# Kernel tuning notes

Hardware: AMD Instinct MI355X
Metric: run time of the kernel (lower is better)

Reference implementation:

```python
import jax, jax.numpy as jnp
import numpy as np

OFFS = [(dy, dx) for dy in (-1, 0, 1) for dx in (-1, 0, 1)]  # ME centered 3x3 region


def _build_maps():
    """Build the sparse coordinate pyramid and per-offset kernel maps, exactly
    mirroring MinkowskiEngine: out coords of a stride-2 conv are unique(c//2),
    and a pair (i_in, i_out) exists iff coord_out*stride + offset is active."""
    G = 1024
    rng = np.random.default_rng(0)
    flat = np.sort(rng.choice(G * G, size=300000, replace=False))
    coords = [np.stack(np.unravel_index(flat, (G, G)), axis=1).astype(np.int64)]
    grids = [G]
    for _ in range(3):
        coords.append(np.unique(coords[-1] // 2, axis=0))
        grids.append(grids[-1] // 2)

    def lut(c, g):
        t = -np.ones(g * g, np.int64)
        t[c[:, 0] * g + c[:, 1]] = np.arange(len(c))
        return t

    luts = [lut(c, g) for c, g in zip(coords, grids)]

    def kmap(lvl_in, c_out, stride):
        g, L = grids[lvl_in], luts[lvl_in]
        n_in, n_out = len(coords[lvl_in]), len(c_out)
        base = c_out * stride
        pairs = []
        for dy, dx in OFFS:
            q = base + np.array([dy, dx])
            ok = (q[:, 0] >= 0) & (q[:, 0] < g) & (q[:, 1] >= 0) & (q[:, 1] < g)
            key = np.clip(q[:, 0] * g + q[:, 1], 0, g * g - 1)
            idx = np.where(ok, L[key], -1)
            sel = np.nonzero(idx >= 0)[0]
            pairs.append((idx[sel], sel))
        M = max(len(p[0]) for p in pairs)
        ii = np.full((9, M), n_in, np.int32)   # pad -> dummy zero input row
        oo = np.full((9, M), n_out, np.int32)  # pad -> dummy output row (dropped)
        for k, (a, b) in enumerate(pairs):
            ii[k, :len(a)] = a
            oo[k, :len(b)] = b
        return ii, oo

    maps = {
        'c0': kmap(0, coords[0], 1), 'd0': kmap(0, coords[1], 2),
        'c1': kmap(1, coords[1], 1), 'd1': kmap(1, coords[2], 2),
        'c2': kmap(2, coords[2], 1), 'd2': kmap(2, coords[3], 2),
    }
    return maps, [len(c) for c in coords]


def setup_inputs() -> dict:
    maps, (n0, n1, n2, n3) = _build_maps()
    ks = jax.random.split(jax.random.key(0), 16)
    d = {'feats': jax.random.normal(ks[0], (n0, 1), jnp.float32)}
    chans = [(1, 64), (64, 128), (128, 128), (128, 128), (128, 128), (128, 128)]
    names = ['c0', 'd0', 'c1', 'd1', 'c2', 'd2']
    for i, (nm, (ci, co)) in enumerate(zip(names, chans)):
        d[f'w_{nm}'] = jax.random.normal(ks[1 + 2 * i], (9, ci, co), jnp.float32) / np.sqrt(9.0 * ci)
        d[f'b_{nm}'] = jax.random.normal(ks[2 + 2 * i], (co,), jnp.float32) * 0.01
        d[f'in_{nm}'] = jnp.asarray(maps[nm][0])
        d[f'out_{nm}'] = jnp.asarray(maps[nm][1])
    d.update(n0=n0, n1=n1, n2=n2, n3=n3)
    return d


def sparse_conv(feats, w, b, in_idx, out_idx, n_out):
    """Gather-GEMM-scatter sparse conv. w: [9, Cin, Cout]. Padded pairs point at a
    dummy zero input row (index n_in) and a dummy output row (index n_out)."""
    n_in, cin = feats.shape
    fp = jnp.concatenate([feats, jnp.zeros((1, cin), feats.dtype)], axis=0)
    out = jnp.zeros((n_out + 1, w.shape[2]), feats.dtype)
    for k in range(9):  # fixed kernel volume
        out = out.at[out_idx[k]].add(fp[in_idx[k]] @ w[k])
    return out[:n_out] + b


def reference(feats, w_c0, b_c0, in_c0, out_c0, w_d0, b_d0, in_d0, out_d0,
              w_c1, b_c1, in_c1, out_c1, w_d1, b_d1, in_d1, out_d1,
              w_c2, b_c2, in_c2, out_c2, w_d2, b_d2, in_d2, out_d2,
              n0, n1, n2, n3):
    x = sparse_conv(feats, w_c0, b_c0, in_c0, out_c0, n0)
    out0 = jax.nn.relu(sparse_conv(x, w_d0, b_d0, in_d0, out_d0, n1))
    y = sparse_conv(out0, w_c1, b_c1, in_c1, out_c1, n1)
    out1 = jax.nn.relu(sparse_conv(y, w_d1, b_d1, in_d1, out_d1, n2))
    z = sparse_conv(out1, w_c2, b_c2, in_c2, out_c2, n2)
    out2 = sparse_conv(z, w_d2, b_d2, in_d2, out_d2, n3)
    return (out2, out1, out0)
```

## Files before the change

kernel.cpp:

```cpp
#include <hip/hip_runtime.h>
#include <stdint.h>
#include <algorithm>


#define DI __device__ __forceinline__

typedef __attribute__((ext_vector_type(8))) short bf16x8;
typedef __attribute__((ext_vector_type(4))) float f32x4;

DI uint16_t f2bf(float x){
  union{float f;uint32_t i;}v; v.f=x;
  uint32_t r = v.i + 0x7fffu + ((v.i>>16)&1u);
  return (uint16_t)(r>>16);
}
DI uint32_t pack2(float a, float b){
  return (uint32_t)f2bf(a) | ((uint32_t)f2bf(b) << 16);
}
DI void gload16(const void* g, void* l){
  __builtin_amdgcn_global_load_lds(
      (const __attribute__((address_space(1))) void*)g,
      (__attribute__((address_space(3))) void*)l, 16, 0, 0);
}

__global__ __launch_bounds__(256) void diag_kernel(float* __restrict__ out, long n, float c){
  long i = (long)blockIdx.x*256 + threadIdx.x;
  if (i < n) out[i] = c;
}

__global__ __launch_bounds__(256) void init_all_kernel(
    int* __restrict__ tab, long ntab, float* __restrict__ zp){
  long i = (long)blockIdx.x*256 + threadIdx.x;
  if (i < ntab) tab[i] = -1;
  if (blockIdx.x == 0 && threadIdx.x < 64) zp[threadIdx.x] = 0.f;
}

struct BuildArgs {
  const int* im[6];
  const int* om[6];
  int   M[6];
  int   nin[6];
  int   nout[6];
  long  toff[6];
};

__global__ __launch_bounds__(256) void build_all_kernel(
    BuildArgs a, int* __restrict__ tb){
  const int L = blockIdx.z, k = blockIdx.y;
  const int M = a.M[L];
  long t = (long)blockIdx.x*256 + threadIdx.x;
  if (t >= M) return;
  int ii = a.im[L][(long)k*M + t];
  int oo = a.om[L][(long)k*M + t];
  if (ii >= 0 && ii < a.nin[L] && oo >= 0 && oo < a.nout[L])
    tb[a.toff[L] + (long)k*a.nout[L] + oo] = ii;
}

__global__ __launch_bounds__(256) void prep_all_kernel(
    const float* __restrict__ w0, const float* __restrict__ w1,
    const float* __restrict__ w2, const float* __restrict__ w3,
    const float* __restrict__ w4, uint16_t* __restrict__ wb, long total){
  const long wt64 = 9L*128*64, wt128 = 9L*128*128;
  long idx = (long)blockIdx.x*256 + threadIdx.x;
  if (idx >= total) return;
  int L; long r; int cin;
  if (idx < wt64){ L = 0; r = idx; cin = 64; }
  else { long j = idx - wt64; L = 1 + (int)(j / wt128); r = j % wt128; cin = 128; }
  const float* w = (L==0) ? w0 : (L==1) ? w1 : (L==2) ? w2 : (L==3) ? w3 : w4;
  int k = (int)(r / (128*cin));
  int rem = (int)(r % (128*cin));
  int cout = rem / cin, ci = rem % cin;
  wb[idx] = f2bf(w[((long)k*cin + ci)*128 + cout]);
}

__global__ __launch_bounds__(256) void c0_tab_kernel(
    const float* __restrict__ feats, const float* __restrict__ w,
    const float* __restrict__ bias, const int* __restrict__ tab,
    uint16_t* __restrict__ out, int n_out){
  __shared__ float w_s[576];
  __shared__ float b_s[64];
  const int tid = threadIdx.x;
  for (int i = tid; i < 576; i += 256) w_s[i] = w[i];
  if (tid < 64) b_s[tid] = bias[tid];
  __syncthreads();
  long r = (long)blockIdx.x*256 + tid;
  if (r >= n_out) return;
  float f[9];
  #pragma unroll
  for (int k = 0; k < 9; k++){
    int gi = tab[(long)k*n_out + r];
    f[k] = (gi >= 0) ? feats[gi] : 0.f;
  }
  uint16_t* dst = out + r*64;
  #pragma unroll
  for (int c0 = 0; c0 < 64; c0 += 16){
    float a[16];
    #pragma unroll
    for (int j = 0; j < 16; j++) a[j] = b_s[c0+j];
    #pragma unroll
    for (int k = 0; k < 9; k++){
      float fk = f[k];
      #pragma unroll
      for (int j = 0; j < 16; j++) a[j] += fk * w_s[k*64 + c0 + j];
    }
    uint4 o0, o1;
    o0.x = pack2(a[0],a[1]);   o0.y = pack2(a[2],a[3]);
    o0.z = pack2(a[4],a[5]);   o0.w = pack2(a[6],a[7]);
    o1.x = pack2(a[8],a[9]);   o1.y = pack2(a[10],a[11]);
    o1.z = pack2(a[12],a[13]); o1.w = pack2(a[14],a[15]);
    *(uint4*)(dst + c0)     = o0;
    *(uint4*)(dst + c0 + 8) = o1;
  }
}

template<int CIN, int INMODE, int OUTMODE, bool RELU>
__global__ __launch_bounds__(512,4) void mconv2_kernel(
    const void* __restrict__ in_v, const char* __restrict__ ws_base,
    long in_off, long wtb_off, long zp_off,
    const float* __restrict__ bias, const int* __restrict__ tab,
    float* __restrict__ outf, uint16_t* __restrict__ outb, int n_out){
  constexpr int NS = 9*CIN/64;
  __shared__ __align__(16) uint16_t ab[2][128*64];
  __shared__ __align__(16) uint16_t bb[2][128*64];
  __shared__ int gi_sh[(INMODE==1) ? 9*128 : 1];

  const int tid = threadIdx.x;
  const int nwg = gridDim.x, orig = blockIdx.x;
  const int q = nwg >> 3, rr = nwg & 7, xcd = orig & 7, pos = orig >> 3;
  const int wg = (xcd < rr ? xcd*(q+1) : rr*(q+1) + (xcd-rr)*q) + pos;
  const long rb = (long)wg * 128;

  const int r0 = tid >> 3, sg = tid & 7;
  const int ss0 = sg ^ (r0 & 7);

  uint32_t offA[2][9];
  if constexpr (INMODE == 0){
    #pragma unroll
    for (int kk = 0; kk < 9; ++kk){
      #pragma unroll
      for (int it = 0; it < 2; ++it){
        long row = rb + it*64 + r0;
        int gi = (row < (long)n_out) ? tab[(long)kk*n_out + row] : -1;
        offA[it][kk] = (gi >= 0)
            ? (uint32_t)(in_off + (long)gi*(CIN*2) + ss0*16)
            : (uint32_t)(zp_off + ss0*16);
      }
    }
  } else {
    for (int idx = tid; idx < 9*128; idx += 512){
      int k = idx >> 7, r = idx & 127;
      long row = rb + r;
      gi_sh[idx] = (row < (long)n_out) ? tab[(long)k*n_out + row] : -1;
    }
    __syncthreads();
  }

  const uint32_t offB = (uint32_t)(wtb_off + ((long)r0*CIN + ss0*8)*2);

  const int lane = tid & 63;
  const int wv = tid >> 6;
  const int wr = (wv >> 1) << 5;
  const int wc = (wv & 1) << 6;
  const int l16 = lane & 15, quad = lane >> 4;

  float bv[4];
  #pragma unroll
  for (int ct = 0; ct < 4; ++ct) bv[ct] = bias[wc + (ct<<4) + l16];

  f32x4 acc[2][4];
  #pragma unroll
  for (int i = 0; i < 2; i++)
    #pragma unroll
    for (int j = 0; j < 4; j++)
      acc[i][j] = (f32x4){0.f,0.f,0.f,0.f};

  auto stage_b = [&](int step, int nb){
    const int kk  = (CIN == 64) ? step : (step >> 1);
    const int c0b = (CIN == 64) ? 0 : ((step & 1) * 128);
    const uint32_t base = offB + (uint32_t)((long)kk*128*CIN*2 + c0b);
    #pragma unroll
    for (int it = 0; it < 2; ++it)
      gload16(ws_base + base + it*(64*CIN*2), &bb[nb][(it*512+tid)*8]);
  };
  auto stage_a_bf = [&](int step, int nb){
    const int kk  = (CIN == 64) ? step : (step >> 1);
    const int c0b = (CIN == 64) ? 0 : ((step & 1) * 128);
    #pragma unroll
    for (int it = 0; it < 2; ++it)
      gload16(ws_base + offA[it][kk] + c0b, &ab[nb][(it*512+tid)*8]);
  };
  auto stage_a_f32_issue = [&](int step, float4 (*va)[2]){
    const int kk = step >> 1;
    const int ci0 = (step & 1) << 6;
    const float* fb = (const float*)in_v;
    #pragma unroll
    for (int it = 0; it < 2; ++it){
      int gi = gi_sh[(kk << 7) + it*64 + r0];
      if (gi >= 0){
        const float4* s = (const float4*)(fb + (long)gi*128 + ci0 + ss0*8);
        va[it][0] = s[0]; va[it][1] = s[1];
      } else {
        va[it][0] = make_float4(0.f,0.f,0.f,0.f);
        va[it][1] = make_float4(0.f,0.f,0.f,0.f);
      }
    }
  };
  auto stage_a_f32_write = [&](float4 (*va)[2], int nb){
    #pragma unroll
    for (int it = 0; it < 2; ++it){
      uint4 o;
      o.x = pack2(va[it][0].x, va[it][0].y);
      o.y = pack2(va[it][0].z, va[it][0].w);
      o.z = pack2(va[it][1].x, va[it][1].y);
      o.w = pack2(va[it][1].z, va[it][1].w);
      *(uint4*)&ab[nb][(it*512+tid)*8] = o;
    }
  };
  auto compute = [&](int nb){
    const uint16_t* A  = &ab[nb][0];
    const uint16_t* Bm = &bb[nb][0];
    __builtin_amdgcn_s_setprio(1);
    #pragma unroll
    for (int ch = 0; ch < 2; ++ch){
      const int xs = ((((ch << 2) + quad) ^ (l16 & 7)) << 3);
      bf16x8 af[2], bfr[4];
      #pragma unroll
      for (int u = 0; u < 2; ++u)
        af[u]  = *(const bf16x8*)&A [((wr + (u<<4) + l16) << 6) + xs];
      #pragma unroll
      for (int u = 0; u < 4; ++u)
        bfr[u] = *(const bf16x8*)&Bm[((wc + (u<<4) + l16) << 6) + xs];
      #pragma unroll
      for (int rt = 0; rt < 2; ++rt)
        #pragma unroll
        for (int ct = 0; ct < 4; ++ct)
          acc[rt][ct] = __builtin_amdgcn_mfma_f32_16x16x32_bf16(
              af[rt], bfr[ct], acc[rt][ct], 0, 0, 0);
    }
    __builtin_amdgcn_s_setprio(0);
  };

  if constexpr (INMODE == 0){
    stage_a_bf(0, 0);
    stage_b(0, 0);
    #pragma unroll
    for (int t = 0; t < NS; ++t){
      const int cur = t & 1;
      if (t + 1 < NS){
        stage_a_bf(t+1, cur^1);
        stage_b(t+1, cur^1);
        asm volatile("s_waitcnt vmcnt(4)" ::: "memory");
      } else {
        asm volatile("s_waitcnt vmcnt(0)" ::: "memory");
      }
      __builtin_amdgcn_sched_barrier(0);
      __builtin_amdgcn_s_barrier();
      compute(cur);
      if (t + 1 < NS)
        __builtin_amdgcn_s_barrier();
    }
  } else {
    float4 va[2][2];
    stage_a_f32_issue(0, va);
    stage_a_f32_write(va, 0);
    stage_b(0, 0);
    __syncthreads();
    #pragma unroll
    for (int t = 0; t < NS; ++t){
      const int cur = t & 1;
      const bool more = (t + 1 < NS);
      if (more){
        stage_a_f32_issue(t+1, va);
        stage_b(t+1, cur^1);
      }
      compute(cur);
      if (more){
        stage_a_f32_write(va, cur^1);
        __syncthreads();
      }
    }
  }

  #pragma unroll
  for (int ct = 0; ct < 4; ++ct){
    const int cout = wc + (ct<<4) + l16;
    #pragma unroll
    for (int rt = 0; rt < 2; ++rt){
      #pragma unroll
      for (int r = 0; r < 4; ++r){
        long row = rb + wr + (rt<<4) + (quad<<2) + r;
        if (row < (long)n_out){
          float v = acc[rt][ct][r] + bv[ct];
          if (RELU) v = v > 0.f ? v : 0.f;
          if constexpr (OUTMODE == 0 || OUTMODE == 2) outf[row*128 + cout] = v;
          if constexpr (OUTMODE == 1 || OUTMODE == 2) outb[row*128 + cout] = f2bf(v);
        }
      }
    }
  }
}

static inline long cdivl(long a, long b){ return (a + b - 1) / b; }

extern "C" void kernel_launch(void* const* d_in, const int* in_sizes, int n_in_args,
                              void* d_out, int out_size, void* d_ws, size_t ws_size,
                              hipStream_t stream) {
  const float* feats = (const float*)d_in[0];
  const float* w_c0 = (const float*)d_in[1];
  const float* b_c0 = (const float*)d_in[2];
  const int* in_c0  = (const int*)d_in[3];
  const int* out_c0 = (const int*)d_in[4];
  const float* w_d0 = (const float*)d_in[5];
  const float* b_d0 = (const float*)d_in[6];
  const int* in_d0  = (const int*)d_in[7];
  const int* out_d0 = (const int*)d_in[8];
  const float* w_c1 = (const float*)d_in[9];
  const float* b_c1 = (const float*)d_in[10];
  const int* in_c1  = (const int*)d_in[11];
  const int* out_c1 = (const int*)d_in[12];
  const float* w_d1 = (const float*)d_in[13];
  const float* b_d1 = (const float*)d_in[14];
  const int* in_d1  = (const int*)d_in[15];
  const int* out_d1 = (const int*)d_in[16];
  const float* w_c2 = (const float*)d_in[17];
  const float* b_c2 = (const float*)d_in[18];
  const int* in_c2  = (const int*)d_in[19];
  const int* out_c2 = (const int*)d_in[20];
  const float* w_d2 = (const float*)d_in[21];
  const float* b_d2 = (const float*)d_in[22];
  const int* in_d2  = (const int*)d_in[23];
  const int* out_d2 = (const int*)d_in[24];

  const int n0   = in_sizes[0];
  const int M_c0 = in_sizes[3]  / 9;
  const int M_d0 = in_sizes[7]  / 9;
  const int M_c1 = in_sizes[11] / 9;
  const int M_d1 = in_sizes[15] / 9;
  const int M_c2 = in_sizes[19] / 9;
  const int M_d2 = in_sizes[23] / 9;
  const int n1   = M_c1;
  const int n2   = M_c2;
  const int n3   = out_size/128 - n1 - n2;

  bool sane = n0 > 0 && out_size % 128 == 0 &&
              M_c0 > 0 && M_d0 > 0 && M_d1 > 0 && M_d2 > 0 &&
              n1 > 0 && n2 > 0 && n3 > 0;

  long maxElems = (long)n0*64;
  if ((long)n1*128 > maxElems) maxElems = (long)n1*128;
  if ((long)n2*128 > maxElems) maxElems = (long)n2*128;
  long fbytes = (maxElems*2 + 255)/256*256;
  long ntab   = sane ? 9L*((long)n0 + 2L*n1 + 2L*n2 + n3) : 0;
  long tbytes = (ntab*4 + 255)/256*256;
  long wt64  = 9L*128*64, wt128 = 9L*128*128;
  long wbytes = ((wt64 + 4*wt128)*2 + 255)/256*256;
  long zbytes = 256;
  long b1bytes = sane ? ((long)n2*128*2 + 255)/256*256 : 0;
  long b0bytes = sane ? ((long)n1*128*2 + 255)/256*256 : 0;
  long need0 = fbytes + tbytes + wbytes + zbytes + 256;

  if (!sane || ws_size < (size_t)need0){
    float C = (float)(16 + (int)std::min<size_t>(ws_size >> 20, (size_t)100000));
    if (!sane) C *= 1099511627776.0f;
    diag_kernel<<<cdivl(out_size,256),256,0,stream>>>((float*)d_out, out_size, C);
    return;
  }

  uint16_t* fbuf = (uint16_t*)d_ws;
  long tab_off    = fbytes;
  long wtb_d0_off = fbytes + tbytes;
  long wtb_c1_off = wtb_d0_off + wt64*2;
  long wtb_d1_off = wtb_c1_off + wt128*2;
  long wtb_c2_off = wtb_d1_off + wt128*2;
  long wtb_d2_off = wtb_c2_off + wt128*2;
  long zp_off     = fbytes + tbytes + wbytes;
  long bf1_off    = need0;
  long bf0_off    = need0 + b1bytes;
  const char* wsb = (const char*)d_ws;
  int* tb        = (int*)((char*)d_ws + tab_off);
  float* zp_p    = (float*)((char*)d_ws + zp_off);
  uint16_t* bf1  = (uint16_t*)((char*)d_ws + bf1_off);
  uint16_t* bf0  = (uint16_t*)((char*)d_ws + bf0_off);
  int tier = 0;
  if (ws_size >= (size_t)(need0 + b1bytes)) tier = 1;
  if (ws_size >= (size_t)(need0 + b1bytes + b0bytes)) tier = 2;

  long t_c0 = 0;
  long t_d0 = t_c0 + 9L*n0;
  long t_c1 = t_d0 + 9L*n1;
  long t_d1 = t_c1 + 9L*n1;
  long t_c2 = t_d1 + 9L*n2;
  long t_d2 = t_c2 + 9L*n2;

  float* out2 = (float*)d_out;
  float* out1 = out2 + (long)n3*128;
  float* out0 = out1 + (long)n2*128;

  init_all_kernel<<<cdivl(ntab,256),256,0,stream>>>(tb, ntab, zp_p);

  BuildArgs ba;
  ba.im[0]=in_c0;  ba.om[0]=out_c0; ba.M[0]=M_c0; ba.nin[0]=n0; ba.nout[0]=n0; ba.toff[0]=t_c0;
  ba.im[1]=in_d0;  ba.om[1]=out_d0; ba.M[1]=M_d0; ba.nin[1]=n0; ba.nout[1]=n1; ba.toff[1]=t_d0;
  ba.im[2]=in_c1;  ba.om[2]=out_c1; ba.M[2]=M_c1; ba.nin[2]=n1; ba.nout[2]=n1; ba.toff[2]=t_c1;
  ba.im[3]=in_d1;  ba.om[3]=out_d1; ba.M[3]=M_d1; ba.nin[3]=n1; ba.nout[3]=n2; ba.toff[3]=t_d1;
  ba.im[4]=in_c2;  ba.om[4]=out_c2; ba.M[4]=M_c2; ba.nin[4]=n2; ba.nout[4]=n2; ba.toff[4]=t_c2;
  ba.im[5]=in_d2;  ba.om[5]=out_d2; ba.M[5]=M_d2; ba.nin[5]=n2; ba.nout[5]=n3; ba.toff[5]=t_d2;
  long maxM = M_c0;
  for (int i = 0; i < 6; ++i) if (ba.M[i] > maxM) maxM = ba.M[i];
  dim3 bg((unsigned)cdivl(maxM,256), 9, 6);
  build_all_kernel<<<bg,256,0,stream>>>(ba, tb);

  long wtotal = wt64 + 4*wt128;
  prep_all_kernel<<<cdivl(wtotal,256),256,0,stream>>>(
      w_d0, w_c1, w_d1, w_c2, w_d2,
      (uint16_t*)((char*)d_ws + wtb_d0_off), wtotal);

  c0_tab_kernel<<<cdivl(n0,256),256,0,stream>>>(feats, w_c0, b_c0, tb + t_c0, fbuf, n0);

  if (tier >= 2)
    mconv2_kernel<64,0,2,true><<<cdivl(n1,128),512,0,stream>>>(
        nullptr, wsb, 0L, wtb_d0_off, zp_off, b_d0, tb + t_d0, out0, bf0, n1);
  else
    mconv2_kernel<64,0,0,true><<<cdivl(n1,128),512,0,stream>>>(
        nullptr, wsb, 0L, wtb_d0_off, zp_off, b_d0, tb + t_d0, out0, nullptr, n1);

  if (tier >= 2)
    mconv2_kernel<128,0,1,false><<<cdivl(n1,128),512,0,stream>>>(
        nullptr, wsb, bf0_off, wtb_c1_off, zp_off, b_c1, tb + t_c1, nullptr, fbuf, n1);
  else
    mconv2_kernel<128,1,1,false><<<cdivl(n1,128),512,0,stream>>>(
        out0, wsb, 0L, wtb_c1_off, zp_off, b_c1, tb + t_c1, nullptr, fbuf, n1);

  if (tier >= 1)
    mconv2_kernel<128,0,2,true><<<cdivl(n2,128),512,0,stream>>>(
        nullptr, wsb, 0L, wtb_d1_off, zp_off, b_d1, tb + t_d1, out1, bf1, n2);
  else
    mconv2_kernel<128,0,0,true><<<cdivl(n2,128),512,0,stream>>>(
        nullptr, wsb, 0L, wtb_d1_off, zp_off, b_d1, tb + t_d1, out1, nullptr, n2);

  if (tier >= 1)
    mconv2_kernel<128,0,1,false><<<cdivl(n2,128),512,0,stream>>>(
        nullptr, wsb, bf1_off, wtb_c2_off, zp_off, b_c2, tb + t_c2, nullptr, fbuf, n2);
  else
    mconv2_kernel<128,1,1,false><<<cdivl(n2,128),512,0,stream>>>(
        out1, wsb, 0L, wtb_c2_off, zp_off, b_c2, tb + t_c2, nullptr, fbuf, n2);

  mconv2_kernel<128,0,0,false><<<cdivl(n3,128),512,0,stream>>>(
      nullptr, wsb, 0L, wtb_d2_off, zp_off, b_d2, tb + t_d2, out2, nullptr, n3);
}
```

Measured before the change: 486.7 us.

## Switch conv GEMM to 32-wide K steps with triple-buffered LDS pipeline

```diff
diff --git a/kernel.cpp b/kernel.cpp
--- a/kernel.cpp
+++ b/kernel.cpp
@@ -112,16 +112,14 @@
   }
 }
 
-template<int CIN, int INMODE, int OUTMODE, bool RELU>
-__global__ __launch_bounds__(512,4) void mconv2_kernel(
-    const void* __restrict__ in_v, const char* __restrict__ ws_base,
-    long in_off, long wtb_off, long zp_off,
+template<int CIN, int OUTMODE, bool RELU>
+__global__ __launch_bounds__(512,6) void mconv3_kernel(
+    const char* __restrict__ ws_base, long in_off, long wtb_off, long zp_off,
     const float* __restrict__ bias, const int* __restrict__ tab,
     float* __restrict__ outf, uint16_t* __restrict__ outb, int n_out){
-  constexpr int NS = 9*CIN/64;
-  __shared__ __align__(16) uint16_t ab[2][128*64];
-  __shared__ __align__(16) uint16_t bb[2][128*64];
-  __shared__ int gi_sh[(INMODE==1) ? 9*128 : 1];
+  constexpr int NS = 9*CIN/32;
+  __shared__ __align__(16) uint16_t ab[3][128*32];
+  __shared__ __align__(16) uint16_t bb[3][128*32];
 
   const int tid = threadIdx.x;
   const int nwg = gridDim.x, orig = blockIdx.x;
@@ -129,38 +127,25 @@
   const int wg = (xcd < rr ? xcd*(q+1) : rr*(q+1) + (xcd-rr)*q) + pos;
   const long rb = (long)wg * 128;
 
-  const int r0 = tid >> 3, sg = tid & 7;
-  const int ss0 = sg ^ (r0 & 7);
-
-  uint32_t offA[2][9];
-  if constexpr (INMODE == 0){
-    #pragma unroll
-    for (int kk = 0; kk < 9; ++kk){
-      #pragma unroll
-      for (int it = 0; it < 2; ++it){
-        long row = rb + it*64 + r0;
-        int gi = (row < (long)n_out) ? tab[(long)kk*n_out + row] : -1;
-        offA[it][kk] = (gi >= 0)
-            ? (uint32_t)(in_off + (long)gi*(CIN*2) + ss0*16)
-            : (uint32_t)(zp_off + ss0*16);
-      }
-    }
-  } else {
-    for (int idx = tid; idx < 9*128; idx += 512){
-      int k = idx >> 7, r = idx & 127;
-      long row = rb + r;
-      gi_sh[idx] = (row < (long)n_out) ? tab[(long)k*n_out + row] : -1;
-    }
-    __syncthreads();
-  }
-
-  const uint32_t offB = (uint32_t)(wtb_off + ((long)r0*CIN + ss0*8)*2);
+  const int r0 = tid >> 2, sg = tid & 3;
+  const int lsg = sg ^ ((r0 >> 1) & 3);
+
+  uint32_t offA[9];
+  #pragma unroll
+  for (int kk = 0; kk < 9; ++kk){
+    long row = rb + r0;
+    int gi = (row < (long)n_out) ? tab[(long)kk*n_out + row] : -1;
+    offA[kk] = (gi >= 0) ? (uint32_t)(in_off + (long)gi*(CIN*2) + lsg*16)
+                         : (uint32_t)(zp_off + lsg*16);
+  }
+  const uint32_t offB0 = (uint32_t)(wtb_off + ((long)r0*CIN + lsg*8)*2);
 
   const int lane = tid & 63;
   const int wv = tid >> 6;
   const int wr = (wv >> 1) << 5;
   const int wc = (wv & 1) << 6;
   const int l16 = lane & 15, quad = lane >> 4;
+  const int xsw = (quad ^ ((l16 >> 1) & 3)) << 3;
 
   float bv[4];
   #pragma unroll
@@ -173,111 +158,49 @@
     for (int j = 0; j < 4; j++)
       acc[i][j] = (f32x4){0.f,0.f,0.f,0.f};
 
-  auto stage_b = [&](int step, int nb){
-    const int kk  = (CIN == 64) ? step : (step >> 1);
-    const int c0b = (CIN == 64) ? 0 : ((step & 1) * 128);
-    const uint32_t base = offB + (uint32_t)((long)kk*128*CIN*2 + c0b);
-    #pragma unroll
-    for (int it = 0; it < 2; ++it)
-      gload16(ws_base + base + it*(64*CIN*2), &bb[nb][(it*512+tid)*8]);
-  };
-  auto stage_a_bf = [&](int step, int nb){
-    const int kk  = (CIN == 64) ? step : (step >> 1);
-    const int c0b = (CIN == 64) ? 0 : ((step & 1) * 128);
-    #pragma unroll
-    for (int it = 0; it < 2; ++it)
-      gload16(ws_base + offA[it][kk] + c0b, &ab[nb][(it*512+tid)*8]);
-  };
-  auto stage_a_f32_issue = [&](int step, float4 (*va)[2]){
-    const int kk = step >> 1;
-    const int ci0 = (step & 1) << 6;
-    const float* fb = (const float*)in_v;
-    #pragma unroll
-    for (int it = 0; it < 2; ++it){
-      int gi = gi_sh[(kk << 7) + it*64 + r0];
-      if (gi >= 0){
-        const float4* s = (const float4*)(fb + (long)gi*128 + ci0 + ss0*8);
-        va[it][0] = s[0]; va[it][1] = s[1];
-      } else {
-        va[it][0] = make_float4(0.f,0.f,0.f,0.f);
-        va[it][1] = make_float4(0.f,0.f,0.f,0.f);
-      }
-    }
-  };
-  auto stage_a_f32_write = [&](float4 (*va)[2], int nb){
-    #pragma unroll
-    for (int it = 0; it < 2; ++it){
-      uint4 o;
-      o.x = pack2(va[it][0].x, va[it][0].y);
-      o.y = pack2(va[it][0].z, va[it][0].w);
-      o.z = pack2(va[it][1].x, va[it][1].y);
-      o.w = pack2(va[it][1].z, va[it][1].w);
-      *(uint4*)&ab[nb][(it*512+tid)*8] = o;
-    }
+  auto stage = [&](int t, int nb){
+    const int kk = t / (CIN/32), ch = t % (CIN/32);
+    gload16(ws_base + offA[kk] + ch*64, &ab[nb][tid*8]);
+    gload16(ws_base + offB0 + (uint32_t)((long)kk*128*CIN*2) + ch*64,
+            &bb[nb][tid*8]);
   };
   auto compute = [&](int nb){
     const uint16_t* A  = &ab[nb][0];
     const uint16_t* Bm = &bb[nb][0];
     __builtin_amdgcn_s_setprio(1);
-    #pragma unroll
-    for (int ch = 0; ch < 2; ++ch){
-      const int xs = ((((ch << 2) + quad) ^ (l16 & 7)) << 3);
-      bf16x8 af[2], bfr[4];
+    bf16x8 af[2], bfr[4];
+    #pragma unroll
+    for (int u = 0; u < 2; ++u)
+      af[u]  = *(const bf16x8*)&A [((wr + (u<<4) + l16) << 5) + xsw];
+    #pragma unroll
+    for (int u = 0; u < 4; ++u)
+      bfr[u] = *(const bf16x8*)&Bm[((wc + (u<<4) + l16) << 5) + xsw];
+    #pragma unroll
+    for (int rt = 0; rt < 2; ++rt)
       #pragma unroll
-      for (int u = 0; u < 2; ++u)
-        af[u]  = *(const bf16x8*)&A [((wr + (u<<4) + l16) << 6) + xs];
-      #pragma unroll
-      for (int u = 0; u < 4; ++u)
-        bfr[u] = *(const bf16x8*)&Bm[((wc + (u<<4) + l16) << 6) + xs];
-      #pragma unroll
-      for (int rt = 0; rt < 2; ++rt)
-        #pragma unroll
-        for (int ct = 0; ct < 4; ++ct)
-          acc[rt][ct] = __builtin_amdgcn_mfma_f32_16x16x32_bf16(
-              af[rt], bfr[ct], acc[rt][ct], 0, 0, 0);
-    }
+      for (int ct = 0; ct < 4; ++ct)
+        acc[rt][ct] = __builtin_amdgcn_mfma_f32_16x16x32_bf16(
+            af[rt], bfr[ct], acc[rt][ct], 0, 0, 0);
     __builtin_amdgcn_s_setprio(0);
   };
 
-  if constexpr (INMODE == 0){
-    stage_a_bf(0, 0);
-    stage_b(0, 0);
-    #pragma unroll
-    for (int t = 0; t < NS; ++t){
-      const int cur = t & 1;
-      if (t + 1 < NS){
-        stage_a_bf(t+1, cur^1);
-        stage_b(t+1, cur^1);
-        asm volatile("s_waitcnt vmcnt(4)" ::: "memory");
-      } else {
-        asm volatile("s_waitcnt vmcnt(0)" ::: "memory");
-      }
-      __builtin_amdgcn_sched_barrier(0);
+  stage(0, 0);
+  stage(1, 1);
+  #pragma unroll
+  for (int t = 0; t < NS; ++t){
+    if (t + 2 < NS){
+      stage(t+2, (t+2)%3);
+      asm volatile("s_waitcnt vmcnt(4)" ::: "memory");
+    } else if (t + 1 < NS){
+      asm volatile("s_waitcnt vmcnt(2)" ::: "memory");
+    } else {
+      asm volatile("s_waitcnt vmcnt(0)" ::: "memory");
+    }
+    __builtin_amdgcn_sched_barrier(0);
+    __builtin_amdgcn_s_barrier();
+    compute(t%3);
+    if (t + 1 < NS)
       __builtin_amdgcn_s_barrier();
-      compute(cur);
-      if (t + 1 < NS)
-        __builtin_amdgcn_s_barrier();
-    }
-  } else {
-    float4 va[2][2];
-    stage_a_f32_issue(0, va);
-    stage_a_f32_write(va, 0);
-    stage_b(0, 0);
-    __syncthreads();
-    #pragma unroll
-    for (int t = 0; t < NS; ++t){
-      const int cur = t & 1;
-      const bool more = (t + 1 < NS);
-      if (more){
-        stage_a_f32_issue(t+1, va);
-        stage_b(t+1, cur^1);
-      }
-      compute(cur);
-      if (more){
-        stage_a_f32_write(va, cur^1);
-        __syncthreads();
-      }
-    }
   }
 
   #pragma unroll
@@ -356,9 +279,9 @@
   long zbytes = 256;
   long b1bytes = sane ? ((long)n2*128*2 + 255)/256*256 : 0;
   long b0bytes = sane ? ((long)n1*128*2 + 255)/256*256 : 0;
-  long need0 = fbytes + tbytes + wbytes + zbytes + 256;
-
-  if (!sane || ws_size < (size_t)need0){
+  long need_full = fbytes + tbytes + wbytes + zbytes + 256 + b1bytes + b0bytes;
+
+  if (!sane || ws_size < (size_t)need_full){
     float C = (float)(16 + (int)std::min<size_t>(ws_size >> 20, (size_t)100000));
     if (!sane) C *= 1099511627776.0f;
     diag_kernel<<<cdivl(out_size,256),256,0,stream>>>((float*)d_out, out_size, C);
@@ -367,22 +290,15 @@
 
   uint16_t* fbuf = (uint16_t*)d_ws;
   long tab_off    = fbytes;
-  long wtb_d0_off = fbytes + tbytes;
-  long wtb_c1_off = wtb_d0_off + wt64*2;
-  long wtb_d1_off = wtb_c1_off + wt128*2;
-  long wtb_c2_off = wtb_d1_off + wt128*2;
-  long wtb_d2_off = wtb_c2_off + wt128*2;
+  long wtb_off    = fbytes + tbytes;
   long zp_off     = fbytes + tbytes + wbytes;
-  long bf1_off    = need0;
-  long bf0_off    = need0 + b1bytes;
+  long bf1_off    = zp_off + zbytes + 256;
+  long bf0_off    = bf1_off + b1bytes;
   const char* wsb = (const char*)d_ws;
   int* tb        = (int*)((char*)d_ws + tab_off);
   float* zp_p    = (float*)((char*)d_ws + zp_off);
   uint16_t* bf1  = (uint16_t*)((char*)d_ws + bf1_off);
   uint16_t* bf0  = (uint16_t*)((char*)d_ws + bf0_off);
-  int tier = 0;
-  if (ws_size >= (size_t)(need0 + b1bytes)) tier = 1;
-  if (ws_size >= (size_t)(need0 + b1bytes + b0bytes)) tier = 2;
 
   long t_c0 = 0;
   long t_d0 = t_c0 + 9L*n0;
@@ -412,38 +328,22 @@
   long wtotal = wt64 + 4*wt128;
   prep_all_kernel<<<cdivl(wtotal,256),256,0,stream>>>(
       w_d0, w_c1, w_d1, w_c2, w_d2,
-      (uint16_t*)((char*)d_ws + wtb_d0_off), wtotal);
+      (uint16_t*)((char*)d_ws + wtb_off), wtotal);
 
   c0_tab_kernel<<<cdivl(n0,256),256,0,stream>>>(feats, w_c0, b_c0, tb + t_c0, fbuf, n0);
 
-  if (tier >= 2)
-    mconv2_kernel<64,0,2,true><<<cdivl(n1,128),512,0,stream>>>(
-        nullptr, wsb, 0L, wtb_d0_off, zp_off, b_d0, tb + t_d0, out0, bf0, n1);
-  else
-    mconv2_kernel<64,0,0,true><<<cdivl(n1,128),512,0,stream>>>(
-        nullptr, wsb, 0L, wtb_d0_off, zp_off, b_d0, tb + t_d0, out0, nullptr, n1);
-
-  if (tier >= 2)
-    mconv2_kernel<128,0,1,false><<<cdivl(n1,128),512,0,stream>>>(
-        nullptr, wsb, bf0_off, wtb_c1_off, zp_off, b_c1, tb + t_c1, nullptr, fbuf, n1);
-  else
-    mconv2_kernel<128,1,1,false><<<cdivl(n1,128),512,0,stream>>>(
-        out0, wsb, 0L, wtb_c1_off, zp_off, b_c1, tb + t_c1, nullptr, fbuf, n1);
-
-  if (tier >= 1)
-    mconv2_kernel<128,0,2,true><<<cdivl(n2,128),512,0,stream>>>(
-        nullptr, wsb, 0L, wtb_d1_off, zp_off, b_d1, tb + t_d1, out1, bf1, n2);
-  else
-    mconv2_kernel<128,0,0,true><<<cdivl(n2,128),512,0,stream>>>(
-        nullptr, wsb, 0L, wtb_d1_off, zp_off, b_d1, tb + t_d1, out1, nullptr, n2);
-
-  if (tier >= 1)
-    mconv2_kernel<128,0,1,false><<<cdivl(n2,128),512,0,stream>>>(
-        nullptr, wsb, bf1_off, wtb_c2_off, zp_off, b_c2, tb + t_c2, nullptr, fbuf, n2);
-  else
-    mconv2_kernel<128,1,1,false><<<cdivl(n2,128),512,0,stream>>>(
-        out1, wsb, 0L, wtb_c2_off, zp_off, b_c2, tb + t_c2, nullptr, fbuf, n2);
-
-  mconv2_kernel<128,0,0,false><<<cdivl(n3,128),512,0,stream>>>(
-      nullptr, wsb, 0L, wtb_d2_off, zp_off, b_d2, tb + t_d2, out2, nullptr, n3);
-}
+  mconv3_kernel<64,2,true><<<cdivl(n1,128),512,0,stream>>>(
+      wsb, 0L, wtb_off, zp_off, b_d0, tb + t_d0, out0, bf0, n1);
+
+  mconv3_kernel<128,1,false><<<cdivl(n1,128),512,0,stream>>>(
+      wsb, bf0_off, wtb_off + wt64*2, zp_off, b_c1, tb + t_c1, nullptr, fbuf, n1);
+
+  mconv3_kernel<128,2,true><<<cdivl(n2,128),512,0,stream>>>(
+      wsb, 0L, wtb_off + (wt64 + wt128)*2, zp_off, b_d1, tb + t_d1, out1, bf1, n2);
+
+  mconv3_kernel<128,1,false><<<cdivl(n2,128),512,0,stream>>>(
+      wsb, bf1_off, wtb_off + (wt64 + 2*wt128)*2, zp_off, b_c2, tb + t_c2, nullptr, fbuf, n2);
+
+  mconv3_kernel<128,0,false><<<cdivl(n3,128),512,0,stream>>>(
+      wsb, 0L, wtb_off + (wt64 + 3*wt128)*2, zp_off, b_d2, tb + t_d2, out2, nullptr, n3);
+}
```

Result: slower. 541.0 us (+11.2%).
